# Kernel optimization log

Hardware: AMD Instinct MI355X
Metric: run time of the kernel (lower is better)

## Reference

```python
import jax, jax.numpy as jnp
import numpy as np

ORDER = 3  # polynomial filter order


def _sketch_conv(x, A, W, b, coeffs):
    # z = A @ (x W + b); out = sum_d coeffs[d-1] * z**d  (Horner-free power accumulation)
    z = A @ (x @ W + b)            # [N, out_c]
    p = z
    acc = coeffs[0] * z
    for d in range(1, ORDER):      # small fixed loop over polynomial order
        p = p * z
        acc = acc + coeffs[d] * p
    return acc


def setup_inputs() -> dict:
    key = jax.random.key(0)
    ks = jax.random.split(key, 12)
    N, C_IN, C_H, C_OUT = 8192, 128, 64, 40
    nf_mats = jax.random.normal(ks[0], (N, C_IN), dtype=jnp.float32)
    # scale by 1/sqrt(N) so polynomial powers stay O(1)
    conv_mats = jax.random.normal(ks[1], (N, N), dtype=jnp.float32) / np.float32(np.sqrt(N))
    def lin(k, fi, fo):
        kw, kb = jax.random.split(k)
        W = jax.random.normal(kw, (fi, fo), dtype=jnp.float32) / np.float32(np.sqrt(fi))
        b = jax.random.normal(kb, (fo,), dtype=jnp.float32) * np.float32(0.01)
        return W, b
    W1, b1 = lin(ks[2], C_IN, C_H)
    W2, b2 = lin(ks[3], C_H, C_H)
    W3, b3 = lin(ks[4], C_H, C_OUT)
    base = jnp.array([1.0, 0.0, 0.0], dtype=jnp.float32)
    c1 = base + jax.random.normal(ks[5], (ORDER,), dtype=jnp.float32) * 0.05
    c2 = base + jax.random.normal(ks[6], (ORDER,), dtype=jnp.float32) * 0.05
    c3 = base + jax.random.normal(ks[7], (ORDER,), dtype=jnp.float32) * 0.05
    return {"nf_mats": nf_mats, "conv_mats": conv_mats,
            "W1": W1, "b1": b1, "c1": c1,
            "W2": W2, "b2": b2, "c2": c2,
            "W3": W3, "b3": b3, "c3": c3}


def reference(nf_mats, conv_mats, W1, b1, c1, W2, b2, c2, W3, b3, c3):
    # SketchGCN eval-mode forward: batchnorm=False, dropout inactive.
    x = _sketch_conv(nf_mats, conv_mats, W1, b1, c1)      # first layer
    x = x + _sketch_conv(x, conv_mats, W2, b2, c2)        # residual middle layer
    return _sketch_conv(x, conv_mats, W3, b3, c3)         # output layer
```

## Files before the change

kernel.cpp:

```cpp
#include <hip/hip_runtime.h>
#include <stdint.h>

typedef __bf16 bf16x8 __attribute__((ext_vector_type(8)));
typedef float f32x4 __attribute__((ext_vector_type(4)));

using gvoid = const __attribute__((address_space(1))) void;
using lvoid = __attribute__((address_space(3))) void;

__device__ __forceinline__ unsigned short f2bf(float f) {
    union { float f; unsigned u; } x; x.f = f;
    unsigned u = x.u;
    u += 0x7FFFu + ((u >> 16) & 1u);
    return (unsigned short)(u >> 16);
}
__device__ __forceinline__ unsigned pack2(float lo, float hi) {
    return ((unsigned)f2bf(hi) << 16) | (unsigned)f2bf(lo);
}

__global__ __launch_bounds__(256) void convert_bf16(const float* __restrict__ in,
                                                    unsigned short* __restrict__ out,
                                                    int n8) {
    int idx = blockIdx.x * 256 + threadIdx.x;
    int stride = gridDim.x * 256;
    const float4* in4 = (const float4*)in;
    uint4* out8 = (uint4*)out;
    for (int i = idx; i < n8; i += stride) {
        float4 a = in4[2 * i], b = in4[2 * i + 1];
        uint4 o;
        o.x = pack2(a.x, a.y);
        o.y = pack2(a.z, a.w);
        o.z = pack2(b.x, b.y);
        o.w = pack2(b.z, b.w);
        out8[i] = o;
    }
}

template <int CIN>
__global__ __launch_bounds__(256) void small_gemm(const float* __restrict__ X,
                                                  const float* __restrict__ W,
                                                  const float* __restrict__ b,
                                                  int cout,
                                                  unsigned short* __restrict__ Yt) {
    __shared__ float Xs[32 * (CIN + 1)];
    __shared__ float Ws[CIN * 64];
    __shared__ float bs[64];
    const int t = threadIdx.x;
    const int i0 = blockIdx.x * 32;

    for (int e = t; e < 32 * CIN; e += 256) {
        int r = e / CIN, c = e % CIN;
        Xs[r * (CIN + 1) + c] = X[(size_t)(i0 + r) * CIN + c];
    }
    for (int e = t; e < CIN * 64; e += 256) {
        int k = e >> 6, j = e & 63;
        Ws[e] = (j < cout) ? W[k * cout + j] : 0.0f;
    }
    if (t < 64) bs[t] = (t < cout) ? b[t] : 0.0f;
    __syncthreads();

    const int i = t & 31;
    const int jg = t >> 5;
    float acc[8];
#pragma unroll
    for (int jj = 0; jj < 8; ++jj) acc[jj] = 0.0f;

    for (int k = 0; k < CIN; ++k) {
        float xv = Xs[i * (CIN + 1) + k];
        const float4* wr = (const float4*)&Ws[k * 64 + jg * 8];
        float4 w0 = wr[0], w1 = wr[1];
        acc[0] += xv * w0.x; acc[1] += xv * w0.y;
        acc[2] += xv * w0.z; acc[3] += xv * w0.w;
        acc[4] += xv * w1.x; acc[5] += xv * w1.y;
        acc[6] += xv * w1.z; acc[7] += xv * w1.w;
    }
#pragma unroll
    for (int jj = 0; jj < 8; ++jj) {
        int j = jg * 8 + jj;
        Yt[(size_t)j * 8192 + i0 + i] = f2bf(acc[jj] + bs[j]);
    }
}

__global__ __launch_bounds__(256, 3)
void big_gemm(const unsigned short* __restrict__ Ab,
              const unsigned short* __restrict__ Yt,
              float* __restrict__ P) {
    __shared__ unsigned short As[3][64 * 64];
    __shared__ unsigned short Bs[3][64 * 64];
    const int t = threadIdx.x;
    const int lane = t & 63, wid = t >> 6;
    const int lane15 = lane & 15, lane4 = lane >> 4;
    const int wm = wid >> 1, wn = wid & 1;
    const int row0 = blockIdx.x * 64;
    const int kbase = blockIdx.y * 1024;

    f32x4 acc[2][2];
    const f32x4 z4 = {0.f, 0.f, 0.f, 0.f};
#pragma unroll
    for (int m = 0; m < 2; ++m)
#pragma unroll
        for (int n = 0; n < 2; ++n) acc[m][n] = z4;

    auto stage = [&](int slot, int kt) {
#pragma unroll
        for (int ii = 0; ii < 2; ++ii) {
            int p = ii * 256 + wid * 64 + lane;
            int r = p >> 3;
            int c = (p & 7) ^ (r & 7);
            const unsigned short* gp = Ab + (size_t)(row0 + r) * 8192 + (kt + c * 8);
            unsigned short* lp = &As[slot][(ii * 256 + wid * 64) * 8];
            __builtin_amdgcn_global_load_lds((gvoid*)gp, (lvoid*)lp, 16, 0, 0);
        }
#pragma unroll
        for (int ii = 0; ii < 2; ++ii) {
            int q = ii * 256 + wid * 64 + lane;
            int n = q >> 3;
            int c = (q & 7) ^ (n & 7);
            const unsigned short* gp = Yt + (size_t)n * 8192 + (kt + c * 8);
            unsigned short* lp = &Bs[slot][(ii * 256 + wid * 64) * 8];
            __builtin_amdgcn_global_load_lds((gvoid*)gp, (lvoid*)lp, 16, 0, 0);
        }
    };

    const int NIT = 16;
    stage(0, kbase);
    int cur = 0, nxt = 1;
    for (int tt = 0; tt < NIT; ++tt) {
        if (tt + 1 < NIT) {
            stage(nxt, kbase + (tt + 1) * 64);
            asm volatile("s_waitcnt vmcnt(4)\n\ts_barrier" ::: "memory");
        } else {
            asm volatile("s_waitcnt vmcnt(0)\n\ts_barrier" ::: "memory");
        }
#pragma unroll
        for (int ks = 0; ks < 2; ++ks) {
            bf16x8 af[2], bfr[2];
#pragma unroll
            for (int m = 0; m < 2; ++m) {
                int r = wm * 32 + m * 16 + lane15;
                int c = ks * 4 + lane4;
                af[m] = *(const bf16x8*)&As[cur][((r << 3) | (c ^ (r & 7))) << 3];
            }
#pragma unroll
            for (int n = 0; n < 2; ++n) {
                int rn = wn * 32 + n * 16 + lane15;
                int c = ks * 4 + lane4;
                bfr[n] = *(const bf16x8*)&Bs[cur][((rn << 3) | (c ^ (rn & 7))) << 3];
            }
#pragma unroll
            for (int m = 0; m < 2; ++m)
#pragma unroll
                for (int n = 0; n < 2; ++n)
                    acc[m][n] = __builtin_amdgcn_mfma_f32_16x16x32_bf16(
                        af[m], bfr[n], acc[m][n], 0, 0, 0);
        }
        cur = (cur == 2) ? 0 : cur + 1;
        nxt = (nxt == 2) ? 0 : nxt + 1;
    }

    float* Po = P + (size_t)blockIdx.y * (8192 * 64);
#pragma unroll
    for (int m = 0; m < 2; ++m) {
        int r = row0 + wm * 32 + m * 16 + lane4 * 4;
#pragma unroll
        for (int n = 0; n < 2; ++n) {
            int cc = wn * 32 + n * 16 + lane15;
#pragma unroll
            for (int q = 0; q < 4; ++q)
                Po[(size_t)(r + q) * 64 + cc] = acc[m][n][q];
        }
    }
}

template <int MODE>
__global__ __launch_bounds__(256) void fused_reduce(const float* __restrict__ P,
                                                    const float* __restrict__ cf,
                                                    const float* __restrict__ Wn,
                                                    const float* __restrict__ bn,
                                                    int cout,
                                                    float* __restrict__ X1,
                                                    unsigned short* __restrict__ Yt) {
    __shared__ float Xs[64 * 33];
    __shared__ float Ws[64 * 64];
    __shared__ float bs[64];
    const int t = threadIdx.x;
    const int i0 = blockIdx.x * 32;
    const int NT4 = 8192 * 64 / 4;
    const float4* P4 = (const float4*)P;
    float4* X14 = (float4*)X1;

    for (int e = t; e < 64 * 64; e += 256) {
        int k = e >> 6, j = e & 63;
        Ws[e] = (j < cout) ? Wn[k * cout + j] : 0.0f;
    }
    if (t < 64) bs[t] = (t < cout) ? bn[t] : 0.0f;
    const float c0 = cf[0], c1 = cf[1], c2 = cf[2];

#pragma unroll
    for (int s = 0; s < 2; ++s) {
        int e4 = s * 256 + t;
        int i = e4 >> 4, jc = e4 & 15;
        int base4 = (i0 + i) * 16 + jc;
        float4 z = {0.f, 0.f, 0.f, 0.f};
#pragma unroll
        for (int ks = 0; ks < 8; ++ks) {
            float4 p = P4[(size_t)ks * NT4 + base4];
            z.x += p.x; z.y += p.y; z.z += p.z; z.w += p.w;
        }
        float4 v;
        v.x = z.x * (c0 + z.x * (c1 + z.x * c2));
        v.y = z.y * (c0 + z.y * (c1 + z.y * c2));
        v.z = z.z * (c0 + z.z * (c1 + z.z * c2));
        v.w = z.w * (c0 + z.w * (c1 + z.w * c2));
        if (MODE == 0) {
            X14[base4] = v;
        } else {
            float4 xr = X14[base4];
            v.x += xr.x; v.y += xr.y; v.z += xr.z; v.w += xr.w;
        }
        Xs[(jc * 4 + 0) * 33 + i] = v.x;
        Xs[(jc * 4 + 1) * 33 + i] = v.y;
        Xs[(jc * 4 + 2) * 33 + i] = v.z;
        Xs[(jc * 4 + 3) * 33 + i] = v.w;
    }
    __syncthreads();

    const int i = t & 31;
    const int jg = t >> 5;
    float acc[8];
#pragma unroll
    for (int jj = 0; jj < 8; ++jj) acc[jj] = 0.0f;
    for (int k = 0; k < 64; ++k) {
        float xv = Xs[k * 33 + i];
        const float4* wr = (const float4*)&Ws[k * 64 + jg * 8];
        float4 w0 = wr[0], w1 = wr[1];
        acc[0] += xv * w0.x; acc[1] += xv * w0.y;
        acc[2] += xv * w0.z; acc[3] += xv * w0.w;
        acc[4] += xv * w1.x; acc[5] += xv * w1.y;
        acc[6] += xv * w1.z; acc[7] += xv * w1.w;
    }
#pragma unroll
    for (int jj = 0; jj < 8; ++jj) {
        int j = jg * 8 + jj;
        Yt[(size_t)j * 8192 + i0 + i] = f2bf(acc[jj] + bs[j]);
    }
}

__global__ void reduce_out(const float* __restrict__ P, const float* __restrict__ cf,
                           float* __restrict__ out) {
    int e4 = blockIdx.x * 256 + threadIdx.x;
    const int NT4 = 8192 * 64 / 4;
    const float4* P4 = (const float4*)P;
    float4 z = {0.f, 0.f, 0.f, 0.f};
#pragma unroll
    for (int ks = 0; ks < 8; ++ks) {
        float4 p = P4[(size_t)ks * NT4 + e4];
        z.x += p.x; z.y += p.y; z.z += p.z; z.w += p.w;
    }
    float c0 = cf[0], c1 = cf[1], c2 = cf[2];
    float4 v;
    v.x = z.x * (c0 + z.x * (c1 + z.x * c2));
    v.y = z.y * (c0 + z.y * (c1 + z.y * c2));
    v.z = z.z * (c0 + z.z * (c1 + z.z * c2));
    v.w = z.w * (c0 + z.w * (c1 + z.w * c2));
    int i = e4 >> 4, jc = e4 & 15;
    if (jc < 10) ((float4*)out)[i * 10 + jc] = v;
}

extern "C" void kernel_launch(void* const* d_in, const int* in_sizes, int n_in,
                              void* d_out, int out_size, void* d_ws, size_t ws_size,
                              hipStream_t stream) {
    const float* nf   = (const float*)d_in[0];
    const float* Amat = (const float*)d_in[1];
    const float* W1   = (const float*)d_in[2];
    const float* b1   = (const float*)d_in[3];
    const float* c1   = (const float*)d_in[4];
    const float* W2   = (const float*)d_in[5];
    const float* b2   = (const float*)d_in[6];
    const float* c2   = (const float*)d_in[7];
    const float* W3   = (const float*)d_in[8];
    const float* b3   = (const float*)d_in[9];
    const float* c3   = (const float*)d_in[10];
    float* out = (float*)d_out;

    char* ws = (char*)d_ws;
    unsigned short* Abf = (unsigned short*)(ws);
    unsigned short* Yt  = (unsigned short*)(ws + 134217728);
    float* X1           = (float*)(ws + 135266304);
    float* Pp           = (float*)(ws + 137363456);

    convert_bf16<<<2048, 256, 0, stream>>>(Amat, Abf, 8192 * 8192 / 8);
    small_gemm<128><<<256, 256, 0, stream>>>(nf, W1, b1, 64, Yt);

    big_gemm<<<dim3(128, 8), 256, 0, stream>>>(Abf, Yt, Pp);
    fused_reduce<0><<<256, 256, 0, stream>>>(Pp, c1, W2, b2, 64, X1, Yt);

    big_gemm<<<dim3(128, 8), 256, 0, stream>>>(Abf, Yt, Pp);
    fused_reduce<1><<<256, 256, 0, stream>>>(Pp, c2, W3, b3, 40, X1, Yt);

    big_gemm<<<dim3(128, 8), 256, 0, stream>>>(Abf, Yt, Pp);
    reduce_out<<<512, 256, 0, stream>>>(Pp, c3, out);
}
```

Baseline: 212.2 us.

## Fuse fp32-to-bf16 conversion of A into the first big GEMM

New measurement: 214.5 us. No clear change (+1.1%).

```diff
diff --git a/kernel.cpp b/kernel.cpp
--- a/kernel.cpp
+++ b/kernel.cpp
@@ -15,24 +15,6 @@
 }
 __device__ __forceinline__ unsigned pack2(float lo, float hi) {
     return ((unsigned)f2bf(hi) << 16) | (unsigned)f2bf(lo);
-}
-
-__global__ __launch_bounds__(256) void convert_bf16(const float* __restrict__ in,
-                                                    unsigned short* __restrict__ out,
-                                                    int n8) {
-    int idx = blockIdx.x * 256 + threadIdx.x;
-    int stride = gridDim.x * 256;
-    const float4* in4 = (const float4*)in;
-    uint4* out8 = (uint4*)out;
-    for (int i = idx; i < n8; i += stride) {
-        float4 a = in4[2 * i], b = in4[2 * i + 1];
-        uint4 o;
-        o.x = pack2(a.x, a.y);
-        o.y = pack2(a.z, a.w);
-        o.z = pack2(b.x, b.y);
-        o.w = pack2(b.z, b.w);
-        out8[i] = o;
-    }
 }
 
 template <int CIN>
@@ -80,12 +62,129 @@
     }
 }
 
-__global__ __launch_bounds__(256, 3)
+__global__ __launch_bounds__(256, 4)
+void gemm_conv(const float* __restrict__ Afp,
+               unsigned short* __restrict__ Ab,
+               const unsigned short* __restrict__ Yt,
+               float* __restrict__ P) {
+    __shared__ unsigned short As[2][64 * 64];
+    __shared__ unsigned short Bs[2][64 * 64];
+    const int t = threadIdx.x;
+    const int lane = t & 63, wid = t >> 6;
+    const int lane15 = lane & 15, lane4 = lane >> 4;
+    const int wm = wid >> 1, wn = wid & 1;
+    const int row0 = blockIdx.x * 64;
+    const int kbase = blockIdx.y * 1024;
+
+    f32x4 acc[2][2];
+    const f32x4 z4 = {0.f, 0.f, 0.f, 0.f};
+#pragma unroll
+    for (int m = 0; m < 2; ++m)
+#pragma unroll
+        for (int n = 0; n < 2; ++n) acc[m][n] = z4;
+
+    float4 ra[2][2];
+    const int p0 = t, p1 = 256 + t;
+    const int r0 = p0 >> 3, c0 = p0 & 7, r1 = p1 >> 3, c1 = p1 & 7;
+
+    auto loadA = [&](int kt) {
+        const float* g0 = Afp + (size_t)(row0 + r0) * 8192 + kt + c0 * 8;
+        const float* g1 = Afp + (size_t)(row0 + r1) * 8192 + kt + c1 * 8;
+        ra[0][0] = *(const float4*)g0; ra[0][1] = *(const float4*)(g0 + 4);
+        ra[1][0] = *(const float4*)g1; ra[1][1] = *(const float4*)(g1 + 4);
+    };
+    auto writeA = [&](int slot, int kt) {
+        uint4 ch0, ch1;
+        ch0.x = pack2(ra[0][0].x, ra[0][0].y); ch0.y = pack2(ra[0][0].z, ra[0][0].w);
+        ch0.z = pack2(ra[0][1].x, ra[0][1].y); ch0.w = pack2(ra[0][1].z, ra[0][1].w);
+        ch1.x = pack2(ra[1][0].x, ra[1][0].y); ch1.y = pack2(ra[1][0].z, ra[1][0].w);
+        ch1.z = pack2(ra[1][1].x, ra[1][1].y); ch1.w = pack2(ra[1][1].z, ra[1][1].w);
+        *(uint4*)&As[slot][((r0 << 3) | (c0 ^ (r0 & 7))) << 3] = ch0;
+        *(uint4*)&As[slot][((r1 << 3) | (c1 ^ (r1 & 7))) << 3] = ch1;
+        *(uint4*)&Ab[(size_t)(row0 + r0) * 8192 + kt + c0 * 8] = ch0;
+        *(uint4*)&Ab[(size_t)(row0 + r1) * 8192 + kt + c1 * 8] = ch1;
+    };
+    auto stageB = [&](int slot, int kt) {
+#pragma unroll
+        for (int ii = 0; ii < 2; ++ii) {
+            int q = ii * 256 + wid * 64 + lane;
+            int n = q >> 3;
+            int c = (q & 7) ^ (n & 7);
+            const unsigned short* gp = Yt + (size_t)n * 8192 + (kt + c * 8);
+            unsigned short* lp = &Bs[slot][(ii * 256 + wid * 64) * 8];
+            __builtin_amdgcn_global_load_lds((gvoid*)gp, (lvoid*)lp, 16, 0, 0);
+        }
+    };
+    auto compute = [&](int slot) {
+#pragma unroll
+        for (int ks = 0; ks < 2; ++ks) {
+            bf16x8 af[2], bfr[2];
+#pragma unroll
+            for (int m = 0; m < 2; ++m) {
+                int r = wm * 32 + m * 16 + lane15;
+                int c = ks * 4 + lane4;
+                af[m] = *(const bf16x8*)&As[slot][((r << 3) | (c ^ (r & 7))) << 3];
+            }
+#pragma unroll
+            for (int n = 0; n < 2; ++n) {
+                int rn = wn * 32 + n * 16 + lane15;
+                int c = ks * 4 + lane4;
+                bfr[n] = *(const bf16x8*)&Bs[slot][((rn << 3) | (c ^ (rn & 7))) << 3];
+            }
+#pragma unroll
+            for (int m = 0; m < 2; ++m)
+#pragma unroll
+                for (int n = 0; n < 2; ++n)
+                    acc[m][n] = __builtin_amdgcn_mfma_f32_16x16x32_bf16(
+                        af[m], bfr[n], acc[m][n], 0, 0, 0);
+        }
+    };
+
+    loadA(kbase);
+    stageB(0, kbase);
+    asm volatile("s_waitcnt vmcnt(2)" ::: "memory");
+    writeA(0, kbase);
+    asm volatile("s_waitcnt lgkmcnt(0)" ::: "memory");
+
+    const int NIT = 16;
+    for (int tt = 0; tt < NIT; ++tt) {
+        if (tt + 1 < NIT) {
+            const int kt1 = kbase + (tt + 1) * 64;
+            loadA(kt1);
+            stageB((tt + 1) & 1, kt1);
+            asm volatile("s_waitcnt vmcnt(8)\n\ts_barrier" ::: "memory");
+        } else {
+            asm volatile("s_waitcnt vmcnt(0)\n\ts_barrier" ::: "memory");
+        }
+        compute(tt & 1);
+        if (tt + 1 < NIT) {
+            asm volatile("s_waitcnt vmcnt(2)" ::: "memory");
+            writeA((tt + 1) & 1, kbase + (tt + 1) * 64);
+            asm volatile("s_waitcnt lgkmcnt(0)" ::: "memory");
+        }
+        asm volatile("s_barrier" ::: "memory");
+    }
+
+    float* Po = P + (size_t)blockIdx.y * (8192 * 64);
+#pragma unroll
+    for (int m = 0; m < 2; ++m) {
+        int r = row0 + wm * 32 + m * 16 + lane4 * 4;
+#pragma unroll
+        for (int n = 0; n < 2; ++n) {
+            int cc = wn * 32 + n * 16 + lane15;
+#pragma unroll
+            for (int q = 0; q < 4; ++q)
+                Po[(size_t)(r + q) * 64 + cc] = acc[m][n][q];
+        }
+    }
+}
+
+__global__ __launch_bounds__(256, 4)
 void big_gemm(const unsigned short* __restrict__ Ab,
               const unsigned short* __restrict__ Yt,
               float* __restrict__ P) {
-    __shared__ unsigned short As[3][64 * 64];
-    __shared__ unsigned short Bs[3][64 * 64];
+    __shared__ unsigned short As[2][64 * 64];
+    __shared__ unsigned short Bs[2][64 * 64];
     const int t = threadIdx.x;
     const int lane = t & 63, wid = t >> 6;
     const int lane15 = lane & 15, lane4 = lane >> 4;
@@ -121,12 +220,11 @@
         }
     };
 
+    stage(0, kbase);
     const int NIT = 16;
-    stage(0, kbase);
-    int cur = 0, nxt = 1;
     for (int tt = 0; tt < NIT; ++tt) {
         if (tt + 1 < NIT) {
-            stage(nxt, kbase + (tt + 1) * 64);
+            stage((tt + 1) & 1, kbase + (tt + 1) * 64);
             asm volatile("s_waitcnt vmcnt(4)\n\ts_barrier" ::: "memory");
         } else {
             asm volatile("s_waitcnt vmcnt(0)\n\ts_barrier" ::: "memory");
@@ -138,13 +236,13 @@
             for (int m = 0; m < 2; ++m) {
                 int r = wm * 32 + m * 16 + lane15;
                 int c = ks * 4 + lane4;
-                af[m] = *(const bf16x8*)&As[cur][((r << 3) | (c ^ (r & 7))) << 3];
+                af[m] = *(const bf16x8*)&As[tt & 1][((r << 3) | (c ^ (r & 7))) << 3];
             }
 #pragma unroll
             for (int n = 0; n < 2; ++n) {
                 int rn = wn * 32 + n * 16 + lane15;
                 int c = ks * 4 + lane4;
-                bfr[n] = *(const bf16x8*)&Bs[cur][((rn << 3) | (c ^ (rn & 7))) << 3];
+                bfr[n] = *(const bf16x8*)&Bs[tt & 1][((rn << 3) | (c ^ (rn & 7))) << 3];
             }
 #pragma unroll
             for (int m = 0; m < 2; ++m)
@@ -153,8 +251,7 @@
                     acc[m][n] = __builtin_amdgcn_mfma_f32_16x16x32_bf16(
                         af[m], bfr[n], acc[m][n], 0, 0, 0);
         }
-        cur = (cur == 2) ? 0 : cur + 1;
-        nxt = (nxt == 2) ? 0 : nxt + 1;
+        asm volatile("s_barrier" ::: "memory");
     }
 
     float* Po = P + (size_t)blockIdx.y * (8192 * 64);
@@ -288,10 +385,9 @@
     float* X1           = (float*)(ws + 135266304);
     float* Pp           = (float*)(ws + 137363456);
 
-    convert_bf16<<<2048, 256, 0, stream>>>(Amat, Abf, 8192 * 8192 / 8);
     small_gemm<128><<<256, 256, 0, stream>>>(nf, W1, b1, 64, Yt);
 
-    big_gemm<<<dim3(128, 8), 256, 0, stream>>>(Abf, Yt, Pp);
+    gemm_conv<<<dim3(128, 8), 256, 0, stream>>>(Amat, Abf, Yt, Pp);
     fused_reduce<0><<<256, 256, 0, stream>>>(Pp, c1, W2, b2, 64, X1, Yt);
 
     big_gemm<<<dim3(128, 8), 256, 0, stream>>>(Abf, Yt, Pp);
```
